# Performance work log

Measured on AMD Instinct MI355X. Metric: run time of the kernel, lower is better.

The kernel has to match this reference:

```python
import jax, jax.numpy as jnp
import numpy as np

NEG_SLOPE = 0.2

def gat_layer(x, src, dst, W, al, ar, b):
    # x: (N, F_in); W: (F_in, H*D); al/ar: (H, D); b: (H, D)
    N = x.shape[0]
    H, D = al.shape
    feat = (x @ W).reshape(N, H, D)                      # (N,H,D)
    el = jnp.sum(feat * al, axis=-1)                     # (N,H) src-side scores
    er = jnp.sum(feat * ar, axis=-1)                     # (N,H) dst-side scores
    e = jax.nn.leaky_relu(el[src] + er[dst], NEG_SLOPE)  # (E,H)
    # edge softmax over incoming edges of each dst node (numerically stable)
    m = jax.ops.segment_max(e, dst, num_segments=N)      # (N,H)
    m = jnp.where(jnp.isfinite(m), m, 0.0)               # guard isolated nodes
    ex = jnp.exp(e - m[dst])                             # (E,H)
    denom = jax.ops.segment_sum(ex, dst, num_segments=N) # (N,H)
    alpha = ex / jnp.maximum(denom[dst], 1e-30)          # (E,H)
    msg = alpha[:, :, None] * feat[src]                  # (E,H,D) gather + weight
    out = jax.ops.segment_sum(msg, dst, num_segments=N)  # (N,H,D) scatter-add
    return out + b[None]                                 # bias per head


def setup_inputs() -> dict:
    key = jax.random.key(0)
    ks = jax.random.split(key, 12)
    N, E, F_in, Dh = 100000, 1600000, 128, 64
    H1 = 2
    inp = {}
    inp['in_feat'] = jax.random.normal(ks[0], (N, F_in), dtype=jnp.float32)
    inp['src'] = jax.random.randint(ks[1], (E,), 0, N, dtype=jnp.int32)
    inp['dst'] = jax.random.randint(ks[2], (E,), 0, N, dtype=jnp.int32)
    s1 = 1.0 / np.sqrt(F_in)
    inp['W1'] = jax.random.normal(ks[3], (F_in, H1 * Dh), dtype=jnp.float32) * s1
    inp['al1'] = jax.random.normal(ks[4], (H1, Dh), dtype=jnp.float32) * 0.1
    inp['ar1'] = jax.random.normal(ks[5], (H1, Dh), dtype=jnp.float32) * 0.1
    inp['b1'] = jnp.zeros((H1, Dh), dtype=jnp.float32)
    s2 = 1.0 / np.sqrt(Dh)
    inp['W2'] = jax.random.normal(ks[6], (Dh, 1 * 2), dtype=jnp.float32) * s2
    inp['al2'] = jax.random.normal(ks[7], (1, 2), dtype=jnp.float32) * 0.1
    inp['ar2'] = jax.random.normal(ks[8], (1, 2), dtype=jnp.float32) * 0.1
    inp['b2'] = jnp.zeros((1, 2), dtype=jnp.float32)
    return inp


def reference(in_feat, src, dst, W1, al1, ar1, b1, W2, al2, ar2, b2):
    num_heads = al1.shape[0]
    h = gat_layer(in_feat, src, dst, W1, al1, ar1, b1)  # (N,2,64)
    h = jnp.sum(h, axis=1) / num_heads                  # head mean
    h = jax.nn.relu(h)
    out = gat_layer(h, src, dst, W2, al2, ar2, b2)      # (N,1,2)
    return out
```

## Files before the change

kernel.cpp:

```cpp
#include <hip/hip_runtime.h>
#include <hip/hip_bf16.h>
#include <hip/hip_fp16.h>

#define LEAKY 0.2f
#define NBMAX 1024
#define CCH   4096
#define SCAP2 3456

typedef _Float16 half8 __attribute__((ext_vector_type(8)));
typedef float f32x4 __attribute__((ext_vector_type(4)));

__device__ __forceinline__ float wave_sum64(float v) {
    #pragma unroll
    for (int m = 32; m > 0; m >>= 1) v += __shfl_xor(v, m, 64);
    return v;
}

__launch_bounds__(256)
__global__ void w1cvt_kernel(const float* __restrict__ W, __half* __restrict__ Wt) {
    int i = blockIdx.x * 256 + threadIdx.x;
    int n = i >> 7, k = i & 127;
    Wt[i] = __float2half(W[k * 128 + n]);
}

__launch_bounds__(256)
__global__ void gemm1_kernel(const float* __restrict__ X, const __half* __restrict__ Wt,
                             const float* __restrict__ al1, const float* __restrict__ ar1,
                             __half* __restrict__ feat_h,
                             float* __restrict__ el1, float* __restrict__ er1, int N) {
    __shared__ __half Al[64 * 136];
    __shared__ __half Wl[128 * 136];
    const int tid = threadIdx.x;
    const int r0 = blockIdx.x * 64;
    {
        int n = tid >> 1, h0 = (tid & 1) * 64;
        const __half* gsrc = Wt + n * 128 + h0;
        __half* ldst = Wl + n * 136 + h0;
        #pragma unroll
        for (int i = 0; i < 8; i++)
            *(uint4*)(ldst + i * 8) = *(const uint4*)(gsrc + i * 8);
    }
    {
        int r = tid >> 2, c0 = (tid & 3) * 32;
        int rr = r0 + r;
        const float* gsrc = X + (size_t)rr * 128 + c0;
        __half* ldst = Al + r * 136 + c0;
        if (rr < N) {
            #pragma unroll
            for (int i = 0; i < 8; i++) {
                float4 v = *(const float4*)(gsrc + i * 4);
                __half2 a = __floats2half2_rn(v.x, v.y);
                __half2 b = __floats2half2_rn(v.z, v.w);
                uint2 pk; pk.x = *(unsigned*)&a; pk.y = *(unsigned*)&b;
                *(uint2*)(ldst + i * 4) = pk;
            }
        } else {
            uint2 z; z.x = 0; z.y = 0;
            #pragma unroll
            for (int i = 0; i < 8; i++) *(uint2*)(ldst + i * 4) = z;
        }
    }
    __syncthreads();
    const int wv = tid >> 6, lane = tid & 63;
    const int lm = lane & 15, lq = lane >> 4;
    f32x4 acc[8];
    #pragma unroll
    for (int t = 0; t < 8; t++) acc[t] = (f32x4){0.f, 0.f, 0.f, 0.f};
    const __half* arow = Al + (wv * 16 + lm) * 136 + lq * 8;
    const __half* brow = Wl + lm * 136 + lq * 8;
    #pragma unroll
    for (int ks = 0; ks < 4; ks++) {
        half8 af = *(const half8*)(arow + ks * 32);
        #pragma unroll
        for (int nt = 0; nt < 8; nt++) {
            half8 bf = *(const half8*)(brow + nt * 16 * 136 + ks * 32);
            acc[nt] = __builtin_amdgcn_mfma_f32_16x16x32_f16(af, bf, acc[nt], 0, 0, 0);
        }
    }
    __syncthreads();
    __half* Cl = Al;
    #pragma unroll
    for (int nt = 0; nt < 8; nt++) {
        #pragma unroll
        for (int r = 0; r < 4; r++) {
            int m = wv * 16 + lq * 4 + r;
            Cl[m * 136 + nt * 16 + lm] = __float2half(acc[nt][r]);
        }
    }
    __syncthreads();
    {
        int r = tid >> 2, c0 = (tid & 3) * 32;
        int rr = r0 + r;
        float pel = 0.f, per = 0.f;
        const __half* crow = Cl + r * 136 + c0;
        if (rr < N) {
            #pragma unroll
            for (int i = 0; i < 4; i++)
                *(uint4*)(feat_h + (size_t)rr * 128 + c0 + i * 8) = *(const uint4*)(crow + i * 8);
            #pragma unroll
            for (int c = 0; c < 32; c++) {
                float fv = __half2float(crow[c]);
                pel += fv * al1[c0 + c];
                per += fv * ar1[c0 + c];
            }
        }
        pel += __shfl_xor(pel, 1, 64);
        per += __shfl_xor(per, 1, 64);
        if ((tid & 1) == 0 && rr < N) {
            int h = (tid >> 1) & 1;
            el1[rr * 2 + h] = pel;
            er1[rr * 2 + h] = per;
        }
    }
}

__launch_bounds__(256)
__global__ void bhist_kernel(const int* __restrict__ dst, int* __restrict__ bcount,
                             int E, int NB) {
    __shared__ int hls[NBMAX];
    for (int i = threadIdx.x; i < NB; i += 256) hls[i] = 0;
    __syncthreads();
    int stride = gridDim.x * 256;
    for (int e = blockIdx.x * 256 + threadIdx.x; e < E; e += stride)
        atomicAdd(&hls[dst[e] >> 7], 1);
    __syncthreads();
    for (int i = threadIdx.x; i < NB; i += 256) {
        int c = hls[i];
        if (c) atomicAdd(&bcount[i], c);
    }
}

__launch_bounds__(1024)
__global__ void bscan_kernel(const int* __restrict__ bcount, int* __restrict__ bstart,
                             int* __restrict__ bcursor, int NB) {
    __shared__ int sd[NBMAX];
    int t = threadIdx.x;
    int v = (t < NB) ? bcount[t] : 0;
    sd[t] = v;
    __syncthreads();
    for (int o = 1; o < NBMAX; o <<= 1) {
        int x = (t >= o) ? sd[t - o] : 0;
        __syncthreads();
        sd[t] += x;
        __syncthreads();
    }
    if (t < NB) { int ex = sd[t] - v; bstart[t] = ex; bcursor[t] = ex; }
}

__launch_bounds__(256)
__global__ void bscatter_kernel(const int* __restrict__ src, const int* __restrict__ dst,
                                const float* __restrict__ el1, const float* __restrict__ er1,
                                int* __restrict__ bcursor, uint2* __restrict__ erec,
                                int E, int NB) {
    __shared__ int hls[NBMAX];
    for (int i = threadIdx.x; i < NB; i += 256) hls[i] = 0;
    __syncthreads();
    const int b0 = blockIdx.x * CCH;
    uint2 ureg[16];
    int breg[16];
    #pragma unroll
    for (int k = 0; k < 16; k++) {
        int e = b0 + k * 256 + threadIdx.x;
        if (e < E) {
            int s = src[e], d = dst[e];
            int bk = d >> 7;
            breg[k] = bk;
            float2 lv = *((const float2*)el1 + s);
            float2 rv = *((const float2*)er1 + d);
            float e0 = lv.x + rv.x; e0 = (e0 > 0.f) ? e0 : LEAKY * e0;
            float e1 = lv.y + rv.y; e1 = (e1 > 0.f) ? e1 : LEAKY * e1;
            __half2 w = __floats2half2_rn(__expf(e0), __expf(e1));
            ureg[k].x = ((unsigned)s << 7) | (unsigned)(d & 127);
            ureg[k].y = *(unsigned*)&w;
            atomicAdd(&hls[bk], 1);
        } else breg[k] = -1;
    }
    __syncthreads();
    for (int b = threadIdx.x; b < NB; b += 256) {
        int c = hls[b];
        if (c) hls[b] = atomicAdd(&bcursor[b], c);
    }
    __syncthreads();
    #pragma unroll
    for (int k = 0; k < 16; k++) {
        if (breg[k] >= 0) {
            int p = atomicAdd(&hls[breg[k]], 1);
            erec[p] = ureg[k];
        }
    }
}

__launch_bounds__(256)
__global__ void bsort_kernel(const uint2* __restrict__ erec,
                             const int* __restrict__ bstart, const int* __restrict__ bcount,
                             uint2* __restrict__ erec2,
                             int* __restrict__ rowstart, int* __restrict__ plen,
                             int* __restrict__ tlen,
                             int N, int NB) {
    __shared__ uint2 sorted[SCAP2];
    __shared__ int cnt[128], prs[129], curs[128];
    const int tid = threadIdx.x;
    const int b = blockIdx.x;
    const int node0 = b << 7;
    const int nd = min(128, N - node0);
    const int ebase = bstart[b];
    int ecnt = bcount[b];
    if (ecnt > SCAP2 - 896) ecnt = SCAP2 - 896;
    const int pbase = ebase + 896 * b;
    if (tid < 128) cnt[tid] = 0;
    __syncthreads();
    for (int j = tid; j < ecnt; j += 256)
        atomicAdd(&cnt[erec[ebase + j].x & 127], 1);
    __syncthreads();
    int pv = 0;
    if (tid < 128) { pv = (cnt[tid] + 7) & ~7; curs[tid] = pv; }
    __syncthreads();
    for (int o = 1; o < 128; o <<= 1) {
        int x = 0;
        if (tid < 128 && tid >= o) x = curs[tid - o];
        __syncthreads();
        if (tid < 128) curs[tid] += x;
        __syncthreads();
    }
    if (tid < 128) prs[tid + 1] = curs[tid];
    if (tid == 0) prs[0] = 0;
    __syncthreads();
    if (tid < 128) curs[tid] = prs[tid + 1] - pv;
    __syncthreads();
    const int pecnt = prs[128];
    for (int j = tid; j < pecnt; j += 256) { sorted[j].x = 0; sorted[j].y = 0; }
    __syncthreads();
    for (int j = tid; j < ecnt; j += 256) {
        uint2 r = erec[ebase + j];
        int p = atomicAdd(&curs[r.x & 127], 1);
        uint2 o2;
        o2.x = (r.x >> 7) << 8;
        o2.y = r.y;
        sorted[p] = o2;
    }
    __syncthreads();
    for (int j = tid; j < pecnt; j += 256) erec2[(size_t)pbase + j] = sorted[j];
    if (tid < nd) {
        rowstart[node0 + tid] = pbase + prs[tid];
        plen[node0 + tid] = prs[tid + 1] - prs[tid];
        tlen[node0 + tid] = cnt[tid];
    }
}

__device__ __forceinline__ void acc_edge(uint2 r, uint2 v, unsigned hsh,
                                         float& acc0, float& acc1,
                                         float& acc2, float& acc3, float& den) {
    unsigned ws = (r.y >> hsh) & 0xffffu;
    den += __half2float(__ushort_as_half((unsigned short)ws));
    asm("v_fma_mix_f32 %0, %1, %2, %0 op_sel:[0,0,0] op_sel_hi:[1,1,0]"
        : "+v"(acc0) : "v"(v.x), "v"(ws));
    asm("v_fma_mix_f32 %0, %1, %2, %0 op_sel:[1,0,0] op_sel_hi:[1,1,0]"
        : "+v"(acc1) : "v"(v.x), "v"(ws));
    asm("v_fma_mix_f32 %0, %1, %2, %0 op_sel:[0,0,0] op_sel_hi:[1,1,0]"
        : "+v"(acc2) : "v"(v.y), "v"(ws));
    asm("v_fma_mix_f32 %0, %1, %2, %0 op_sel:[1,0,0] op_sel_hi:[1,1,0]"
        : "+v"(acc3) : "v"(v.y), "v"(ws));
}

__launch_bounds__(256)
__global__ void agg1_kernel(const char* __restrict__ fh, const uint2* __restrict__ erec2,
                            const float* __restrict__ b1, const float* __restrict__ W2,
                            const float* __restrict__ ar2,
                            const int* __restrict__ rowstart, const int* __restrict__ plen,
                            float* __restrict__ feat2, float* __restrict__ er2, int N) {
    int wid = (blockIdx.x * blockDim.x + threadIdx.x) >> 6;
    int lane = threadIdx.x & 63;
    if (wid >= N) return;
    const int len   = __builtin_amdgcn_readfirstlane(plen[wid]);
    const int rbase = __builtin_amdgcn_readfirstlane(rowstart[wid]);
    const uint2* __restrict__ rp = erec2 + rbase;
    const int l5 = lane & 31;
    const int sub = lane >> 5;
    const unsigned hsh = (l5 < 16) ? 0u : 16u;
    const unsigned lofs = (unsigned)l5 * 8u;
    float acc0 = 0.f, acc1 = 0.f, acc2 = 0.f, acc3 = 0.f, den = 0.f;

#define LDR(R, g) do { const uint2* _p = rp + ((g) * 8 + sub);                     \
        R[0] = _p[0]; R[1] = _p[2]; R[2] = _p[4]; R[3] = _p[6]; } while (0)
#define GTH(V, R) do {                                                             \
        V[0] = *(const uint2*)(fh + (R[0].x + lofs));                              \
        V[1] = *(const uint2*)(fh + (R[1].x + lofs));                              \
        V[2] = *(const uint2*)(fh + (R[2].x + lofs));                              \
        V[3] = *(const uint2*)(fh + (R[3].x + lofs)); } while (0)
#define ACC(R, V) do {                                                             \
        acc_edge(R[0], V[0], hsh, acc0, acc1, acc2, acc3, den);                    \
        acc_edge(R[1], V[1], hsh, acc0, acc1, acc2, acc3, den);                    \
        acc_edge(R[2], V[2], hsh, acc0, acc1, acc2, acc3, den);                    \
        acc_edge(R[3], V[3], hsh, acc0, acc1, acc2, acc3, den); } while (0)

    const int n8 = len >> 3;
    if (n8 > 0) {
        uint2 ra[4], rb[4], va[4], vb[4];
        LDR(ra, 0);
        if (n8 > 1) LDR(rb, 1);
        GTH(va, ra);
        int g = 0;
        while (g + 1 < n8) {
            GTH(vb, rb);
            ACC(ra, va);
            if (g + 2 < n8) LDR(ra, g + 2);
            g++;
            if (g + 1 >= n8) { ACC(rb, vb); g++; break; }
            GTH(va, ra);
            ACC(rb, vb);
            if (g + 2 < n8) LDR(rb, g + 2);
            g++;
        }
        if (g < n8) ACC(ra, va);
    }
#undef LDR
#undef GTH
#undef ACC

    acc0 += __shfl_xor(acc0, 32, 64);
    acc1 += __shfl_xor(acc1, 32, 64);
    acc2 += __shfl_xor(acc2, 32, 64);
    acc3 += __shfl_xor(acc3, 32, 64);
    den  += __shfl_xor(den,  32, 64);
    float inv = 1.f / fmaxf(den, 1e-30f);
    float4 bb = *(const float4*)(b1 + 4 * l5);
    float o0 = acc0 * inv + bb.x;
    float o1 = acc1 * inv + bb.y;
    float o2 = acc2 * inv + bb.z;
    float o3 = acc3 * inv + bb.w;
    float m0 = 0.5f * (o0 + __shfl_xor(o0, 16, 64));
    float m1 = 0.5f * (o1 + __shfl_xor(o1, 16, 64));
    float m2 = 0.5f * (o2 + __shfl_xor(o2, 16, 64));
    float m3 = 0.5f * (o3 + __shfl_xor(o3, 16, 64));
    m0 = fmaxf(m0, 0.f); m1 = fmaxf(m1, 0.f);
    m2 = fmaxf(m2, 0.f); m3 = fmaxf(m3, 0.f);
    const float* wrow = W2 + 8 * (l5 & 15);
    float4 wa = *(const float4*)wrow;
    float4 wb = *(const float4*)(wrow + 4);
    float p0 = m0 * wa.x + m1 * wa.z + m2 * wb.x + m3 * wb.z;
    float p1 = m0 * wa.y + m1 * wa.w + m2 * wb.y + m3 * wb.w;
    float c0 = 0.25f * wave_sum64(p0);
    float c1 = 0.25f * wave_sum64(p1);
    if (lane == 0) {
        float2 f2; f2.x = c0; f2.y = c1;
        *((float2*)feat2 + wid) = f2;
        er2[wid] = c0 * ar2[0] + c1 * ar2[1];
    }
}

__launch_bounds__(256)
__global__ void agg2_kernel(const float* __restrict__ feat2, const float* __restrict__ er2,
                            const float* __restrict__ al2, const float* __restrict__ b2,
                            const int* __restrict__ rowstart, const int* __restrict__ tlen,
                            const uint2* __restrict__ erec2, float* __restrict__ out, int N) {
    int node = (blockIdx.x * 256 + threadIdx.x) >> 4;
    int l4 = threadIdx.x & 15;
    if (node >= N) return;
    const int len = tlen[node];
    const uint2* rp = erec2 + rowstart[node];
    const float ern = er2[node];
    const float al20 = al2[0], al21 = al2[1];
    float den = 0.f, a0 = 0.f, a1 = 0.f;
    for (int j = l4; j < len; j += 16) {
        unsigned key = rp[j].x;
        float2 f = *((const float2*)feat2 + (key >> 8));
        float e = f.x * al20 + f.y * al21 + ern;
        e = (e > 0.f) ? e : LEAKY * e;
        float w = __expf(e);
        den += w;
        a0 += w * f.x;
        a1 += w * f.y;
    }
    #pragma unroll
    for (int m = 1; m < 16; m <<= 1) {
        den += __shfl_xor(den, m, 64);
        a0  += __shfl_xor(a0, m, 64);
        a1  += __shfl_xor(a1, m, 64);
    }
    if (l4 == 0) {
        float inv = 1.f / fmaxf(den, 1e-30f);
        float2 o;
        o.x = a0 * inv + b2[0];
        o.y = a1 * inv + b2[1];
        *((float2*)out + node) = o;
    }
}

extern "C" void kernel_launch(void* const* d_in, const int* in_sizes, int n_in,
                              void* d_out, int out_size, void* d_ws, size_t ws_size,
                              hipStream_t stream) {
    const float* in_feat = (const float*)d_in[0];
    const int*   src     = (const int*)d_in[1];
    const int*   dst     = (const int*)d_in[2];
    const float* W1      = (const float*)d_in[3];
    const float* al1     = (const float*)d_in[4];
    const float* ar1     = (const float*)d_in[5];
    const float* b1      = (const float*)d_in[6];
    const float* W2      = (const float*)d_in[7];
    const float* al2     = (const float*)d_in[8];
    const float* ar2     = (const float*)d_in[9];
    const float* b2      = (const float*)d_in[10];
    float* out = (float*)d_out;

    const int N = in_sizes[0] / 128;
    const int E = in_sizes[1];
    const int NB = (N + 127) >> 7;

    char* ws = (char*)d_ws;
    __half* feat1h = (__half*)ws;
    size_t off = (size_t)N * 128 * 2;
    float* el1 = (float*)(ws + off); off += (size_t)N * 2 * 4;
    float* er1 = (float*)(ws + off); off += (size_t)N * 2 * 4;
    float* feat2 = (float*)(ws + off); off += (size_t)N * 2 * 4;
    float* er2 = (float*)(ws + off); off += (size_t)N * 4;
    int* bcount  = (int*)(ws + off); off += NBMAX * 4;
    int* bstart  = (int*)(ws + off); off += NBMAX * 4;
    int* bcursor = (int*)(ws + off); off += NBMAX * 4;
    int* rowstart = (int*)(ws + off); off += (size_t)N * 4;
    int* plen     = (int*)(ws + off); off += (size_t)N * 4;
    int* tlen     = (int*)(ws + off); off += (size_t)N * 4;
    uint2* erec  = (uint2*)(ws + off); off += (size_t)E * 8;
    uint2* erec2 = (uint2*)(ws + off); off += ((size_t)E + 896 * NB) * 8;
    __half* W1t = (__half*)(ws + off); off += 128 * 128 * 2;
    (void)ws_size; (void)n_in; (void)out_size;

    hipMemsetAsync(bcount, 0, NBMAX * 4, stream);

    w1cvt_kernel<<<64, 256, 0, stream>>>(W1, W1t);
    gemm1_kernel<<<(N + 63) / 64, 256, 0, stream>>>(in_feat, W1t, al1, ar1,
                                                    feat1h, el1, er1, N);

    const int nblkC = (E + CCH - 1) / CCH;
    bhist_kernel<<<nblkC, 256, 0, stream>>>(dst, bcount, E, NB);
    bscan_kernel<<<1, 1024, 0, stream>>>(bcount, bstart, bcursor, NB);
    bscatter_kernel<<<nblkC, 256, 0, stream>>>(src, dst, el1, er1, bcursor, erec, E, NB);
    bsort_kernel<<<NB, 256, 0, stream>>>(erec, bstart, bcount, erec2, rowstart, plen, tlen, N, NB);

    agg1_kernel<<<(N * 64 + 255) / 256, 256, 0, stream>>>(
        (const char*)feat1h, erec2, b1, W2, ar2, rowstart, plen, feat2, er2, N);

    agg2_kernel<<<(N * 16 + 255) / 256, 256, 0, stream>>>(
        feat2, er2, al2, b2, rowstart, tlen, erec2, out, N);
}
```

Measured before the change: 279.4 us.

## Quantize layer-1 features to per-node uint8 with fp16 scale for gather

The GEMM epilogue now quantizes each node's 128 projected features to unsigned 8-bit with one fp16 scale per node, replacing the fp16 feature store. The aggregation kernel gathers 4 bytes per lane plus a scale per edge, dequantizes with an offset correction after the loop, and accumulates in fp32. This halves the bytes moved by the random-access feature gather, which is the main memory cost of agg1. In exchange it adds per-edge scale loads and more ALU work per edge, and loses precision, since 8-bit quantization may exceed the reference tolerance.

```diff
diff --git a/kernel.cpp b/kernel.cpp
--- a/kernel.cpp
+++ b/kernel.cpp
@@ -26,7 +26,7 @@
 __launch_bounds__(256)
 __global__ void gemm1_kernel(const float* __restrict__ X, const __half* __restrict__ Wt,
                              const float* __restrict__ al1, const float* __restrict__ ar1,
-                             __half* __restrict__ feat_h,
+                             unsigned char* __restrict__ feat8, __half* __restrict__ sch,
                              float* __restrict__ el1, float* __restrict__ er1, int N) {
     __shared__ __half Al[64 * 136];
     __shared__ __half Wl[128 * 136];
@@ -94,15 +94,34 @@
         float pel = 0.f, per = 0.f;
         const __half* crow = Cl + r * 136 + c0;
         if (rr < N) {
-            #pragma unroll
-            for (int i = 0; i < 4; i++)
-                *(uint4*)(feat_h + (size_t)rr * 128 + c0 + i * 8) = *(const uint4*)(crow + i * 8);
+            float am = 0.f;
             #pragma unroll
             for (int c = 0; c < 32; c++) {
                 float fv = __half2float(crow[c]);
                 pel += fv * al1[c0 + c];
                 per += fv * ar1[c0 + c];
+                am = fmaxf(am, fabsf(fv));
             }
+            am = fmaxf(am, __shfl_xor(am, 1, 64));
+            am = fmaxf(am, __shfl_xor(am, 2, 64));
+            float s = __half2float(__float2half_rn(fmaxf(am, 1e-8f) * (1.f / 127.5f)));
+            float is = 1.f / s;
+            unsigned pk8[8];
+            #pragma unroll
+            for (int i = 0; i < 8; i++) {
+                unsigned w = 0;
+                #pragma unroll
+                for (int k = 0; k < 4; k++) {
+                    float fv = __half2float(crow[i * 4 + k]);
+                    int q = (int)rintf(fv * is + 127.5f);
+                    q = q < 0 ? 0 : (q > 255 ? 255 : q);
+                    w |= (unsigned)q << (8 * k);
+                }
+                pk8[i] = w;
+            }
+            *(uint4*)(feat8 + (size_t)rr * 128 + c0) = *(const uint4*)&pk8[0];
+            *(uint4*)(feat8 + (size_t)rr * 128 + c0 + 16) = *(const uint4*)&pk8[4];
+            if ((tid & 3) == 0) sch[rr] = __float2half_rn(s);
         }
         pel += __shfl_xor(pel, 1, 64);
         per += __shfl_xor(per, 1, 64);
@@ -247,23 +266,28 @@
     }
 }
 
-__device__ __forceinline__ void acc_edge(uint2 r, uint2 v, unsigned hsh,
-                                         float& acc0, float& acc1,
-                                         float& acc2, float& acc3, float& den) {
+__device__ __forceinline__ void acc_edge8(uint2 r, unsigned v, unsigned short sh, unsigned hsh,
+                                          float& a0, float& a1, float& a2, float& a3,
+                                          float& den, float& csum) {
     unsigned ws = (r.y >> hsh) & 0xffffu;
-    den += __half2float(__ushort_as_half((unsigned short)ws));
-    asm("v_fma_mix_f32 %0, %1, %2, %0 op_sel:[0,0,0] op_sel_hi:[1,1,0]"
-        : "+v"(acc0) : "v"(v.x), "v"(ws));
-    asm("v_fma_mix_f32 %0, %1, %2, %0 op_sel:[1,0,0] op_sel_hi:[1,1,0]"
-        : "+v"(acc1) : "v"(v.x), "v"(ws));
-    asm("v_fma_mix_f32 %0, %1, %2, %0 op_sel:[0,0,0] op_sel_hi:[1,1,0]"
-        : "+v"(acc2) : "v"(v.y), "v"(ws));
-    asm("v_fma_mix_f32 %0, %1, %2, %0 op_sel:[1,0,0] op_sel_hi:[1,1,0]"
-        : "+v"(acc3) : "v"(v.y), "v"(ws));
-}
-
-__launch_bounds__(256)
-__global__ void agg1_kernel(const char* __restrict__ fh, const uint2* __restrict__ erec2,
+    float w = __half2float(__ushort_as_half((unsigned short)ws));
+    den += w;
+    float s = __half2float(__ushort_as_half(sh));
+    float a = w * s;
+    csum += a;
+    float q0 = (float)(v & 0xffu);
+    float q1 = (float)((v >> 8) & 0xffu);
+    float q2 = (float)((v >> 16) & 0xffu);
+    float q3 = (float)(v >> 24);
+    a0 += a * q0;
+    a1 += a * q1;
+    a2 += a * q2;
+    a3 += a * q3;
+}
+
+__launch_bounds__(256)
+__global__ void agg1_kernel(const char* __restrict__ fh, const __half* __restrict__ sch,
+                            const uint2* __restrict__ erec2,
                             const float* __restrict__ b1, const float* __restrict__ W2,
                             const float* __restrict__ ar2,
                             const int* __restrict__ rowstart, const int* __restrict__ plen,
@@ -277,45 +301,56 @@
     const int l5 = lane & 31;
     const int sub = lane >> 5;
     const unsigned hsh = (l5 < 16) ? 0u : 16u;
-    const unsigned lofs = (unsigned)l5 * 8u;
-    float acc0 = 0.f, acc1 = 0.f, acc2 = 0.f, acc3 = 0.f, den = 0.f;
+    const unsigned lofs = (unsigned)l5 * 4u;
+    float acc0 = 0.f, acc1 = 0.f, acc2 = 0.f, acc3 = 0.f, den = 0.f, csum = 0.f;
 
 #define LDR(R, g) do { const uint2* _p = rp + ((g) * 8 + sub);                     \
         R[0] = _p[0]; R[1] = _p[2]; R[2] = _p[4]; R[3] = _p[6]; } while (0)
-#define GTH(V, R) do {                                                             \
-        V[0] = *(const uint2*)(fh + (R[0].x + lofs));                              \
-        V[1] = *(const uint2*)(fh + (R[1].x + lofs));                              \
-        V[2] = *(const uint2*)(fh + (R[2].x + lofs));                              \
-        V[3] = *(const uint2*)(fh + (R[3].x + lofs)); } while (0)
-#define ACC(R, V) do {                                                             \
-        acc_edge(R[0], V[0], hsh, acc0, acc1, acc2, acc3, den);                    \
-        acc_edge(R[1], V[1], hsh, acc0, acc1, acc2, acc3, den);                    \
-        acc_edge(R[2], V[2], hsh, acc0, acc1, acc2, acc3, den);                    \
-        acc_edge(R[3], V[3], hsh, acc0, acc1, acc2, acc3, den); } while (0)
+#define GTH(V, S, R) do {                                                          \
+        V[0] = *(const unsigned*)(fh + ((R[0].x >> 1) + lofs));                    \
+        V[1] = *(const unsigned*)(fh + ((R[1].x >> 1) + lofs));                    \
+        V[2] = *(const unsigned*)(fh + ((R[2].x >> 1) + lofs));                    \
+        V[3] = *(const unsigned*)(fh + ((R[3].x >> 1) + lofs));                    \
+        S[0] = *(const unsigned short*)(sch + (R[0].x >> 8));                      \
+        S[1] = *(const unsigned short*)(sch + (R[1].x >> 8));                      \
+        S[2] = *(const unsigned short*)(sch + (R[2].x >> 8));                      \
+        S[3] = *(const unsigned short*)(sch + (R[3].x >> 8)); } while (0)
+#define ACC(R, V, S) do {                                                          \
+        acc_edge8(R[0], V[0], S[0], hsh, acc0, acc1, acc2, acc3, den, csum);       \
+        acc_edge8(R[1], V[1], S[1], hsh, acc0, acc1, acc2, acc3, den, csum);       \
+        acc_edge8(R[2], V[2], S[2], hsh, acc0, acc1, acc2, acc3, den, csum);       \
+        acc_edge8(R[3], V[3], S[3], hsh, acc0, acc1, acc2, acc3, den, csum); } while (0)
 
     const int n8 = len >> 3;
     if (n8 > 0) {
-        uint2 ra[4], rb[4], va[4], vb[4];
+        uint2 ra[4], rb[4];
+        unsigned va[4], vb[4];
+        unsigned short sa[4], sb[4];
         LDR(ra, 0);
         if (n8 > 1) LDR(rb, 1);
-        GTH(va, ra);
+        GTH(va, sa, ra);
         int g = 0;
         while (g + 1 < n8) {
-            GTH(vb, rb);
-            ACC(ra, va);
+            GTH(vb, sb, rb);
+            ACC(ra, va, sa);
             if (g + 2 < n8) LDR(ra, g + 2);
             g++;
-            if (g + 1 >= n8) { ACC(rb, vb); g++; break; }
-            GTH(va, ra);
-            ACC(rb, vb);
+            if (g + 1 >= n8) { ACC(rb, vb, sb); g++; break; }
+            GTH(va, sa, ra);
+            ACC(rb, vb, sb);
             if (g + 2 < n8) LDR(rb, g + 2);
             g++;
         }
-        if (g < n8) ACC(ra, va);
+        if (g < n8) ACC(ra, va, sa);
     }
 #undef LDR
 #undef GTH
 #undef ACC
+
+    {
+        float corr = 127.5f * csum;
+        acc0 -= corr; acc1 -= corr; acc2 -= corr; acc3 -= corr;
+    }
 
     acc0 += __shfl_xor(acc0, 32, 64);
     acc1 += __shfl_xor(acc1, 32, 64);
@@ -407,8 +442,9 @@
     const int NB = (N + 127) >> 7;
 
     char* ws = (char*)d_ws;
-    __half* feat1h = (__half*)ws;
-    size_t off = (size_t)N * 128 * 2;
+    unsigned char* feat8 = (unsigned char*)ws;
+    size_t off = (size_t)N * 128;
+    __half* scaleh = (__half*)(ws + off); off += (size_t)N * 2;
     float* el1 = (float*)(ws + off); off += (size_t)N * 2 * 4;
     float* er1 = (float*)(ws + off); off += (size_t)N * 2 * 4;
     float* feat2 = (float*)(ws + off); off += (size_t)N * 2 * 4;
@@ -428,7 +464,7 @@
 
     w1cvt_kernel<<<64, 256, 0, stream>>>(W1, W1t);
     gemm1_kernel<<<(N + 63) / 64, 256, 0, stream>>>(in_feat, W1t, al1, ar1,
-                                                    feat1h, el1, er1, N);
+                                                    feat8, scaleh, el1, er1, N);
 
     const int nblkC = (E + CCH - 1) / CCH;
     bhist_kernel<<<nblkC, 256, 0, stream>>>(dst, bcount, E, NB);
@@ -437,7 +473,7 @@
     bsort_kernel<<<NB, 256, 0, stream>>>(erec, bstart, bcount, erec2, rowstart, plen, tlen, N, NB);
 
     agg1_kernel<<<(N * 64 + 255) / 256, 256, 0, stream>>>(
-        (const char*)feat1h, erec2, b1, W2, ar2, rowstart, plen, feat2, er2, N);
+        (const char*)feat8, scaleh, erec2, b1, W2, ar2, rowstart, plen, feat2, er2, N);
 
     agg2_kernel<<<(N * 16 + 255) / 256, 256, 0, stream>>>(
         feat2, er2, al2, b2, rowstart, tlen, erec2, out, N);
```

Measured after the change: 264.7 us. 1.06x faster.
